# Kernel tuning notes

Hardware: AMD Instinct MI355X
Metric: run time of the kernel (lower is better)

Reference implementation:

```python
import jax, jax.numpy as jnp
import numpy as np

MIN_CONF = 0.05          # min_confidence
NMS_IOU = 0.4            # per-class nms iou threshold
POST_IOU = 0.65          # post (cross-class, per-image) nms iou threshold
MAX_OUT = 1000           # nms_max_output_size (also the 'top 1000 boxes' cap)


def _corners(boxes):
    # boxes: [..., 4] (cx, cy, w, h) -> (y1, x1, y2, x2); image w=h=1 since
    # NormalizeBoxes is called without a shape kwarg in the original layer.
    cx, cy, w, h = jnp.moveaxis(boxes, -1, 0)
    return jnp.stack([cy - h / 2, cx - w / 2, cy + h / 2, cx + w / 2], axis=-1)


def _iou_matrix(b):
    # b: [K, 4] (y1, x1, y2, x2) -> [K, K] pairwise IoU
    y1, x1, y2, x2 = b[:, 0], b[:, 1], b[:, 2], b[:, 3]
    area = (y2 - y1) * (x2 - x1)
    ih = jnp.clip(jnp.minimum(y2[:, None], y2[None, :]) - jnp.maximum(y1[:, None], y1[None, :]), 0.0)
    iw = jnp.clip(jnp.minimum(x2[:, None], x2[None, :]) - jnp.maximum(x1[:, None], x1[None, :]), 0.0)
    inter = ih * iw
    union = area[:, None] + area[None, :] - inter
    return inter / jnp.maximum(union, 1e-8)


def _greedy_nms(b, valid, thresh):
    # b: [K,4] corner boxes sorted by descending score; valid: [K] bool.
    # Greedy NMS identical to tf.image.non_max_suppression (suppress IoU > thresh).
    iou = _iou_matrix(b)
    K = b.shape[0]
    idx = jnp.arange(K)
    def body(i, supp):
        active = valid[i] & jnp.logical_not(supp[i])
        return supp | (active & (iou[i] > thresh) & (idx > i))
    supp = jax.lax.fori_loop(0, K, body, jnp.zeros(K, dtype=bool))
    return valid & jnp.logical_not(supp)


def _forward(cls_pred, boxes):
    B, N, C = cls_pred.shape
    K1 = MAX_OUT
    corners = _corners(boxes)                                 # [B, N, 4]

    # --- stage 1: confidence filter + per-(image,class) NMS -----------------
    scores = jnp.transpose(cls_pred, (0, 2, 1))               # [B, C, N]
    masked = jnp.where(scores >= MIN_CONF, scores, -1.0)
    s1, i1 = jax.lax.top_k(masked, K1)                        # [B, C, K1], top-1000 cap
    v1 = s1 >= MIN_CONF
    b1 = jnp.take_along_axis(corners[:, None], i1[..., None], axis=2)  # [B, C, K1, 4]
    keep1 = jax.vmap(lambda bb, vv: _greedy_nms(bb, vv, NMS_IOU))(
        b1.reshape(B * C, K1, 4), v1.reshape(B * C, K1)).reshape(B, C, K1)

    # --- stage 2: per-image cross-class post-NMS ----------------------------
    s2 = jnp.where(keep1, s1, -1.0).reshape(B, C * K1)
    cls_ids = jnp.broadcast_to(jnp.arange(C)[None, :, None], (B, C, K1)).reshape(B, C * K1)
    b2 = b1.reshape(B, C * K1, 4)
    i2 = i1.reshape(B, C * K1)

    K2 = MAX_OUT
    s2t, sel = jax.lax.top_k(s2, K2)                          # [B, K2]
    v2 = s2t >= MIN_CONF
    b2t = jnp.take_along_axis(b2, sel[..., None], axis=1)     # [B, K2, 4]
    cls_t = jnp.take_along_axis(cls_ids, sel, axis=1)         # [B, K2]
    orig_t = jnp.take_along_axis(i2, sel, axis=1)             # [B, K2] anchor index
    keep2 = jax.vmap(lambda bb, vv: _greedy_nms(bb, vv, POST_IOU))(b2t, v2)

    # --- compact kept detections to the front, pad with zeros ---------------
    order = jnp.argsort(jnp.logical_not(keep2).astype(jnp.int32), axis=1)  # stable
    keep_s = jnp.take_along_axis(keep2, order, axis=1)
    conf = jnp.where(keep_s, jnp.take_along_axis(s2t, order, axis=1), 0.0)
    cls_f = jnp.where(keep_s, jnp.take_along_axis(cls_t, order, axis=1), 0).astype(jnp.float32)
    oidx = jnp.take_along_axis(orig_t, order, axis=1)
    raw = jnp.take_along_axis(boxes, oidx[..., None], axis=1)  # original (cx,cy,w,h)
    raw = jnp.where(keep_s[..., None], raw, 0.0)
    out = jnp.concatenate([raw, cls_f[..., None], conf[..., None]], axis=-1)  # [B, K2, 6]
    return jax.lax.stop_gradient(out)


def setup_inputs() -> dict:
    key = jax.random.key(0)
    k1, k2 = jax.random.split(key)
    B, N, C = 8, 100000, 10
    cls_pred = jax.random.uniform(k1, (B, N, C), dtype=jnp.float32)
    boxes = jax.random.uniform(k2, (B, N, 4), dtype=jnp.float32)  # (cx, cy, w, h)
    return {"cls_pred": cls_pred, "boxes": boxes}


def reference(cls_pred, boxes):
    return _forward(cls_pred, boxes)
```

## Files before the change

### kernel.cpp

```cpp
#include <hip/hip_runtime.h>
#include <stdint.h>
#include <string.h>

typedef unsigned int u32;
typedef unsigned long long u64;

#define B_ 8
#define N_ 100000
#define C_ 10
#define K1_ 1000
#define N2_ (C_ * K1_)
#define NBIN 4096
#define CAP 4096
#define CAP_C 2048
#define SEGROWS 256
#define MIN_CONF_F 0.05f
#define NMS_IOU_F 0.4f
#define POST_IOU_F 0.65f
#define T0_F 0.985f

#define TOTAL_F4 (B_ * N_ * C_ / 4)
#define CBLK 512
#define LCAP 512
#define HDRW 84

#define NTILE 136
#define NB_ 34
#define TPB_ 4

static __device__ __forceinline__ u32 next_pow2_ge(u32 x, u32 lo, u32 hi) {
  u32 n = lo;
  while (n < x && n < hi) n <<= 1;
  return n;
}

#define TILE_ID(rt, w) ((rt) * 16 - (((rt) * ((rt) - 1)) >> 1) + ((w) - (rt)))

static __device__ __forceinline__ void prep_write(const float* __restrict__ bb,
                                                  float s, int oi,
                                                  float4* __restrict__ cor,
                                                  int pos) {
  bool v = (s >= MIN_CONF_F);
  float cx = 0.f, cy = 0.f, w = 0.f, h = 0.f;
  if (v) {
    const float4 bp = *(const float4*)(bb + (size_t)oi * 4);
    cx = bp.x; cy = bp.y; w = bp.z; h = bp.w;
  }
  float y1 = cy - h * 0.5f, x1 = cx - w * 0.5f;
  float y2 = cy + h * 0.5f, x2 = cx + w * 0.5f;
  cor[pos] = make_float4(y1, x1, y2, x2);
}

__global__ __launch_bounds__(256) void k_compact(const float* __restrict__ cls,
                                                 u64* __restrict__ cand,
                                                 u32* __restrict__ hdr) {
  __shared__ u32 lcnt[B_ * C_];
  __shared__ u32 lpre[B_ * C_ + 1];
  __shared__ u32 ltot;
  __shared__ u32 lovf;
  __shared__ u64 ekey[LCAP];
  __shared__ u32 emeta[LCAP];

  const int tid = threadIdx.x;
  const u32 bk = blockIdx.x;
  if (tid < B_ * C_) lcnt[tid] = 0;
  if (tid == 0) { ltot = 0; lovf = 0; }
  __syncthreads();

  const u32 lo = bk * ((TOTAL_F4 + CBLK - 1) / CBLK);
  u32 hi = lo + ((TOTAL_F4 + CBLK - 1) / CBLK);
  if (hi > TOTAL_F4) hi = TOTAL_F4;

  const float4* p4 = (const float4*)cls;
// ... 30 lines not shown
  for (int off = 1; off < B_ * C_; off <<= 1) {
    u32 v = 0;
    const bool act = (tid >= off && tid <= B_ * C_);
    if (act) v = lpre[tid - off];
    __syncthreads();
    if (act) lpre[tid] += v;
    __syncthreads();
  }

  u32 tot = ltot;
  if (tot > LCAP) tot = LCAP;
  u64* seg = cand + (size_t)bk * LCAP;
  for (u32 p = tid; p < tot; p += 256) {
    u32 mta = emeta[p];
    u32 slice = mta >> 16;
    u32 rank = mta & 0xFFFFu;
    u32 dst = lpre[slice] + rank;
    if (dst < LCAP) seg[dst] = ekey[p];
  }
  if (tid <= B_ * C_) hdr[bk * HDRW + tid] = lpre[tid];
  if (tid == 0) hdr[bk * HDRW + 81] = lovf;
}

__device__ __forceinline__ void bitonic_sort_desc(u64* buf, u32 n, int tid,
                                                  int bd) {
  for (u32 kk = 2; kk <= n; kk <<= 1) {
    for (u32 j = kk >> 1; j > 0; j >>= 1) {
      for (u32 t = tid; t < (n >> 1); t += bd) {
        u32 i = ((t & ~(j - 1)) << 1) | (t & (j - 1));
        u32 l = i | j;
        u64 a = buf[i], bb = buf[l];
        bool desc = ((i & kk) == 0);
        if (desc ? (a < bb) : (a > bb)) { buf[i] = bb; buf[l] = a; }
      }
      __syncthreads();
    }
  }
}

__global__ __launch_bounds__(1024) void k_sel(const float* __restrict__ cls,
                                              const u64* __restrict__ cand,
                                              const u32* __restrict__ hdr,
                                              float* __restrict__ score1,
                                              int* __restrict__ idx1,
                                              const float* __restrict__ boxes,
                                              float4* __restrict__ cor1,
                                              int do_prep) {
  const int slice = blockIdx.x;
  const int tid = threadIdx.x;
  const int bd = 1024;

  __shared__ u32 hist[NBIN];
  __shared__ u64 buf[CAP];
  __shared__ int sh_b1;
  __shared__ u32 sh_base, sh_T, sh_cnt, sh_ovf;

  u32* cnts = hist;
  u32* starts = hist + 512;
  u32* pre = hist + 1024;

  if (tid == 0) sh_ovf = 0;
  __syncthreads();
// ... 119 lines not shown
        if (l > i) {
          u64 a = buf[i], bb2 = buf[l];
          bool desc = ((i & kk) == 0);
          if (desc ? (a < bb2) : (a > bb2)) { buf[i] = bb2; buf[l] = a; }
        }
      }
      __syncthreads();
    }
  }

  float os = -1.0f; int ooi = 0;
  if (tid < K1_) {
    u64 e = buf[tid];
    u32 k = (u32)(e >> 32);
    if (k != 0) { os = __uint_as_float(k); ooi = (int)(~(u32)e); }
    score1[slice * K1_ + tid] = os;
    idx1[slice * K1_ + tid] = ooi;
  }
  if (do_prep)
    prep_write(boxes + (size_t)(slice / C_) * N_ * 4, os, ooi, cor1,
               (slice << 10) + tid);
}


template <bool STRICT>
static __device__ __forceinline__ bool iou_pred(float inter, float den,
                                                float m1, float m0) {
  float t = __fmul_rn(m1, den);
  float e = __builtin_fmaf(m1, den, -t);
  float r = __builtin_fmaf(m0, den, e);
  float d = __fsub_rn(inter, t);
  return STRICT ? (d > r) : (d >= r);
}

template <bool STRICT>
__global__ __launch_bounds__(256) void k_nms_build(const float4* __restrict__ cor,
                                                   float m1, float m0,
                                                   u64* __restrict__ maskg) {
  __shared__ float4 box4[1024];
  __shared__ float area[1024];
  const int blk = blockIdx.x;
  const int slice = blk / NB_;
  const int sub = blk - slice * NB_;
  const int tid = threadIdx.x, wave = tid >> 6, lane = tid & 63;

  for (int p = tid; p < 1024; p += 256) {
    const float4 c = cor[(slice << 10) + p];
    box4[p] = c;
    area[p] = (c.z - c.x) * (c.w - c.y);
  }
  __syncthreads();

  u64* mg = maskg + (size_t)slice * (NTILE * 64);

  for (int k = wave; k < TPB_; k += 4) {
    const int tt = sub * TPB_ + k;
    if (tt >= NTILE) break;
    int rt = 0, bse = 0;
    while (tt >= bse + (16 - rt)) { bse += 16 - rt; ++rt; }
    const int w = rt + (tt - bse);
    const int row = (rt << 6) | lane;

    const float4 ib = box4[row];
    const float ia = area[row];
    const float4* jcol = &box4[w << 6];
    const float* jarea = &area[w << 6];
    u32 mhi = 0, mlo = 0;
#pragma unroll 8
    for (int j = 63; j >= 32; --j) {
      const float4 jb = jcol[j];
      const float ja = jarea[j];
      float ih = fminf(ib.z, jb.z) - fmaxf(ib.x, jb.x); ih = fmaxf(ih, 0.0f);
      float iw_ = fminf(ib.w, jb.w) - fmaxf(ib.y, jb.y); iw_ = fmaxf(iw_, 0.0f);
      float inter = ih * iw_;
      float den = fmaxf((ia + ja) - inter, 1e-8f);
      bool p_ = iou_pred<STRICT>(inter, den, m1, m0);
      mhi = (mhi << 1) | (p_ ? 1u : 0u);
    }
#pragma unroll 8
    for (int j = 31; j >= 0; --j) {
      const float4 jb = jcol[j];
      const float ja = jarea[j];
      float ih = fminf(ib.z, jb.z) - fmaxf(ib.x, jb.x); ih = fmaxf(ih, 0.0f);
      float iw_ = fminf(ib.w, jb.w) - fmaxf(ib.y, jb.y); iw_ = fmaxf(iw_, 0.0f);
      float inter = ih * iw_;
      float den = fmaxf((ia + ja) - inter, 1e-8f);
      bool p_ = iou_pred<STRICT>(inter, den, m1, m0);
      mlo = (mlo << 1) | (p_ ? 1u : 0u);
    }
    u64 m = ((u64)mhi << 32) | (u64)mlo;
    if (w == rt) m &= (lane == 63) ? 0ull : (~0ull << (lane + 1));
    mg[(tt << 6) + lane] = m;
  }
}

__device__ void scan_core(const u64* __restrict__ mg,
                          const float* __restrict__ scores,
                          u64* __restrict__ keepb) {
  const int tid = threadIdx.x, wv = tid >> 6, lane = tid & 63;

  float s = (tid < K1_) ? scores[tid] : -1.0f;
  const u64 myvalid = __ballot(s >= MIN_CONF_F);

  u64 ext_partial = 0;

#pragma unroll 1
  for (int g = 0; g < 16; ++g) {
    u64 Tg = 0ull;
    if (g <= wv) Tg = mg[(TILE_ID(g, wv) << 6) + lane];
    const u64 nz = __ballot(Tg != 0ull);
    if (wv == g) {
      u64 ext = ext_partial;
      for (int off = 1; off < 64; off <<= 1) {
        u32 lo = (u32)__shfl_xor((int)(u32)ext, off, 64);
        u32 hi = (u32)__shfl_xor((int)(u32)(ext >> 32), off, 64);
        ext |= ((u64)hi << 32) | lo;
      }
      const u32 tlo = (u32)Tg, thi = (u32)(Tg >> 32);
      u64 rem = myvalid & ~ext;
      u64 cand = rem & nz;
      while (cand) {
        int i = __ffsll((long long)cand) - 1;
        cand &= cand - 1;
        if ((rem >> i) & 1ull) {
          u32 rlo = __builtin_amdgcn_readlane(tlo, i);
          u32 rhi = __builtin_amdgcn_readlane(thi, i);
          u64 row = ((u64)rhi << 32) | rlo;
          rem &= ~row;
          cand &= ~row;
        }
      }
      if (lane == 0) keepb[g] = rem;
    }
    __syncthreads();
    if (wv > g) {
      u64 kg = keepb[g];
      if ((kg >> lane) & 1ull) ext_partial |= Tg;
    }
  }
}

__global__ __launch_bounds__(1024) void k_nms_scan1(const u64* __restrict__ maskg,
                                                    const float* __restrict__ score1,
                                                    int* __restrict__ keep1) {
  __shared__ u64 keepb[16];
  const int slice = blockIdx.x;
  scan_core(maskg + (size_t)slice * (NTILE * 64), score1 + slice * K1_, keepb);
  __syncthreads();
  const int p = threadIdx.x;
  if (p < K1_)
    keep1[slice * K1_ + p] = (int)((keepb[p >> 6] >> (p & 63)) & 1ull);
}

__global__ __launch_bounds__(1024) void k_nms_scan2(const u64* __restrict__ maskg,
                                                    const float* __restrict__ sel_score,
                                                    const int* __restrict__ sel_cls,
                                                    const int* __restrict__ sel_orig,
                                                    const float* __restrict__ boxes,
                                                    float* __restrict__ out) {
  __shared__ u64 keepb[16];
  __shared__ short ord[K1_];
  __shared__ int lbase[17];
  __shared__ int ordc;
  const int b = blockIdx.x;
  const int tid = threadIdx.x;
  scan_core(maskg + (size_t)b * (NTILE * 64), sel_score + b * K1_, keepb);
  __syncthreads();

  if (tid == 0) {
    int acc = 0;
    for (int wdx = 0; wdx < 16; ++wdx) {
      lbase[wdx] = acc;
      acc += __popcll(keepb[wdx]);
    }
    lbase[16] = acc;
    ordc = acc;
  }
  __syncthreads();
  if (tid < 16) {
    u64 m = keepb[tid];
    int base = lbase[tid];
    while (m) {
      int bit = __ffsll((long long)m) - 1;
      ord[base++] = (short)((tid << 6) | bit);
      m &= m - 1;
    }
  }
  __syncthreads();

  for (int t = tid; t < K1_ * 6; t += 1024) out[(size_t)b * K1_ * 6 + t] = 0.0f;
  __syncthreads();

  const int cnt = ordc;
  for (int q = tid; q < cnt; q += 1024) {
    int p = ord[q];
    int oi = sel_orig[b * K1_ + p];
    const float4 bp = *(const float4*)(boxes + ((size_t)b * N_ + oi) * 4);
    float* o = out + ((size_t)b * K1_ + q) * 6;
    o[0] = bp.x; o[1] = bp.y; o[2] = bp.z; o[3] = bp.w;
    o[4] = (float)sel_cls[b * K1_ + p];
    o[5] = sel_score[b * K1_ + p];
  }
}

__device__ __forceinline__ void nms_run(const float* __restrict__ scores,
                                        const int* __restrict__ origs,
                                        const float* __restrict__ boxesB,
                                        float thr,
                                        float4* box4, float* area,
                                        u64* mask, u64* validw, u64* keepw) {
  const int tid = threadIdx.x;
  const int wave = tid >> 6, lane = tid & 63;

  {
    const int p = tid;
    float s = (p < K1_) ? scores[p] : -1.0f;
    bool v = (s >= MIN_CONF_F);
    float cx = 0.f, cy = 0.f, w = 0.f, h = 0.f;
    if (v) {
      const float4 bp = *(const float4*)(boxesB + (size_t)origs[p] * 4);
      cx = bp.x; cy = bp.y; w = bp.z; h = bp.w;
    }
    float y1 = cy - h * 0.5f, x1 = cx - w * 0.5f;
    float y2 = cy + h * 0.5f, x2 = cx + w * 0.5f;
    box4[p] = make_float4(y1, x1, y2, x2);
// ... 181 lines not shown
    while (m) {
      int bit = __ffsll((long long)m) - 1;
      ord[base++] = (short)((tid << 6) | bit);
      m &= m - 1;
    }
  }
  __syncthreads();

  for (int t = tid; t < K1_ * 6; t += 1024) out[(size_t)b * K1_ * 6 + t] = 0.0f;
  __syncthreads();

  const int cnt = ordc;
  for (int q = tid; q < cnt; q += 1024) {
    int p = ord[q];
    int oi = sel_orig[b * K1_ + p];
    const float4 bp = *(const float4*)(boxes + ((size_t)b * N_ + oi) * 4);
    float* o = out + ((size_t)b * K1_ + q) * 6;
    o[0] = bp.x; o[1] = bp.y; o[2] = bp.z; o[3] = bp.w;
    o[4] = (float)sel_cls[b * K1_ + p];
    o[5] = sel_score[b * K1_ + p];
  }
}

__device__ __forceinline__ void suffix_select(const u32* __restrict__ hist,
                                              u32* __restrict__ aux,
                                              u32 base, u32 K,
                                              int* out_bin, u32* out_next) {
  const int t = threadIdx.x;
  u32 h0 = hist[4 * t], h1 = hist[4 * t + 1];
  u32 h2 = hist[4 * t + 2], h3 = hist[4 * t + 3];
  aux[t] = h0 + h1 + h2 + h3;
  __syncthreads();
  for (int off = 1; off < 1024; off <<= 1) {
    u32 v = aux[t] + ((t + off < 1024) ? aux[t + off] : 0u);
    __syncthreads();
    aux[t] = v;
    __syncthreads();
  }
  if (t == 0 && base + aux[0] < K) { *out_bin = -1; *out_next = base; }
  u32 up = (t < 1023) ? aux[t + 1] : 0u;
  u32 s3 = h3 + up;
  u32 s2 = h2 + s3;
  u32 s1 = h1 + s2;
  u32 s0 = h0 + s1;
  u32 c0 = base + s0, c1 = base + s1, c2 = base + s2, c3 = base + s3;
  u32 c4 = base + up;
  if (c0 >= K && c1 < K) { *out_bin = 4 * t;     *out_next = c1; }
  if (c1 >= K && c2 < K) { *out_bin = 4 * t + 1; *out_next = c2; }
  if (c2 >= K && c3 < K) { *out_bin = 4 * t + 2; *out_next = c3; }
  if (c3 >= K && c4 < K) { *out_bin = 4 * t + 3; *out_next = c4; }
  __syncthreads();
}

__global__ __launch_bounds__(1024) void k_topk2(const float* __restrict__ score1,
                                                const int* __restrict__ idx1,
                                                const int* __restrict__ keep1,
                                                float* __restrict__ sel_score,
                                                int* __restrict__ sel_cls,
                                                int* __restrict__ sel_orig,
                                                const float* __restrict__ boxes,
                                                float4* __restrict__ cor2,
                                                int do_prep) {
  const int b = blockIdx.x;
  const int tid = threadIdx.x;

  __shared__ u32 hist[NBIN];
  __shared__ u32 aux[1024];
  __shared__ u64 buf[CAP];
  __shared__ int sh_bin;
  __shared__ u32 sh_next;
  __shared__ u32 sh_T, sh_cnt;

  for (int i = tid; i < NBIN; i += 1024) hist[i] = 0;
  __syncthreads();
  for (int f = tid; f < N2_; f += 1024) {
    if (keep1[b * N2_ + f])
      atomicAdd(&hist[__float_as_uint(score1[b * N2_ + f]) >> 19], 1u);
  }
  __syncthreads();
  suffix_select(hist, aux, 0u, (u32)K1_, &sh_bin, &sh_next);
  const int b1 = sh_bin;
  const u32 base = sh_next;

  if (b1 >= 0) {
    for (int i = tid; i < NBIN; i += 1024) hist[i] = 0;
    if (tid == 0) sh_bin = -2;
    __syncthreads();
    for (int f = tid; f < N2_; f += 1024) {
      if (keep1[b * N2_ + f]) {
        u32 k = __float_as_uint(score1[b * N2_ + f]);
        if ((int)(k >> 19) == b1) atomicAdd(&hist[(k >> 7) & 0xFFFu], 1u);
      }
    }
    __syncthreads();
    suffix_select(hist, aux, base, (u32)K1_, &sh_bin, &sh_next);
    if (tid == 0) {
      int b2 = sh_bin;
      sh_T = (b2 >= 0) ? ((((u32)b1) << 19) | (((u32)b2) << 7))
                       : (((u32)b1) << 19);
    }
  } else {
    if (tid == 0) sh_T = 0;
  }
  if (tid == 0) sh_cnt = 0;
  __syncthreads();

  const u32 T = sh_T;
  for (int f = tid; f < N2_; f += 1024) {
    if (keep1[b * N2_ + f]) {
      u32 k = __float_as_uint(score1[b * N2_ + f]);
      if (k >= T) {
        u32 pos = atomicAdd(&sh_cnt, 1u);
        if (pos < CAP) buf[pos] = ((u64)k << 32) | (u32)(~(u32)f);
      }
    }
  }
  __syncthreads();
  u32 m = sh_cnt; if (m > CAP) m = CAP;
  const u32 n = next_pow2_ge(m, 1024u, (u32)CAP);
  for (u32 i = tid; i < n; i += 1024)
    if (i >= m) buf[i] = 0ull;
  __syncthreads();

  bitonic_sort_desc(buf, n, tid, 1024);

  float os = -1.0f; int ooi = 0;
  if (tid < K1_) {
    u64 e = buf[tid];
    u32 k = (u32)(e >> 32);
    float s; int cls, orig;
    if (k == 0) { s = -1.0f; cls = 0; orig = 0; }
    else {
      s = __uint_as_float(k);
      u32 f = ~(u32)e;
      cls = (int)(f / K1_);
      int slot = (int)(f - (u32)cls * K1_);
      orig = idx1[(b * C_ + cls) * K1_ + slot];
    }
    sel_score[b * K1_ + tid] = s;
    sel_cls[b * K1_ + tid] = cls;
    sel_orig[b * K1_ + tid] = orig;
    os = s; ooi = orig;
  }
  if (do_prep)
    prep_write(boxes + (size_t)b * N_ * 4, os, ooi, cor2, (b << 10) + tid);
}

static inline void m_split(float cf, float* m1, float* m0, bool* strict) {
  u32 b; memcpy(&b, &cf, 4);
  u32 nb = b + 1; float cn; memcpy(&cn, &nb, 4);
  double M = ((double)cf + (double)cn) * 0.5;
  *m1 = (float)M;
  *m0 = (float)(M - (double)*m1);
  *strict = ((b & 1u) == 0u);
}

extern "C" void kernel_launch(void* const* d_in, const int* in_sizes, int n_in,
                              void* d_out, int out_size, void* d_ws, size_t ws_size,
                              hipStream_t stream) {
  const float* cls = (const float*)d_in[0];
  const float* boxes = (const float*)d_in[1];
  float* out = (float*)d_out;

  char* ws = (char*)d_ws;
  float* score1    = (float*)(ws);
  int*   idx1      = (int*)(ws + 320000);
  int*   keep1     = (int*)(ws + 640000);
  float* sel_score = (float*)(ws + 960000);
  int*   sel_cls   = (int*)(ws + 992000);
  int*   sel_orig  = (int*)(ws + 1024000);
  u32*   hdr       = (u32*)(ws + 1056000);
  u64*   cand      = (u64*)(ws + 1228032);
  u64*   mask1     = (u64*)(ws + 3325184);
  u64*   mask2     = (u64*)(ws + 3325184);
  float4* cor1     = (float4*)(ws + 8895744);
  float4* cor2     = (float4*)(ws + 8895744);
  const size_t WS_NEED = 10206464;

  const int do_fast = (ws_size >= WS_NEED) ? 1 : 0;

  hipLaunchKernelGGL(k_compact, dim3(CBLK), dim3(256), 0, stream,
                     cls, cand, hdr);
  hipLaunchKernelGGL(k_sel, dim3(B_ * C_), dim3(1024), 0, stream,
                     cls, cand, hdr, score1, idx1, boxes, cor1, do_fast);

  if (do_fast) {
    float m1a, m0a, m1b, m0b; bool sa, sb;
    m_split(NMS_IOU_F, &m1a, &m0a, &sa);
    m_split(POST_IOU_F, &m1b, &m0b, &sb);

    if (sa)
      hipLaunchKernelGGL(k_nms_build<true>, dim3(B_ * C_ * NB_), dim3(256), 0,
                         stream, cor1, m1a, m0a, mask1);
    else
      hipLaunchKernelGGL(k_nms_build<false>, dim3(B_ * C_ * NB_), dim3(256), 0,
                         stream, cor1, m1a, m0a, mask1);
    hipLaunchKernelGGL(k_nms_scan1, dim3(B_ * C_), dim3(1024), 0, stream,
                       mask1, score1, keep1);
    hipLaunchKernelGGL(k_topk2, dim3(B_), dim3(1024), 0, stream,
                       score1, idx1, keep1, sel_score, sel_cls, sel_orig,
                       boxes, cor2, 1);
    if (sb)
      hipLaunchKernelGGL(k_nms_build<true>, dim3(B_ * NB_), dim3(256), 0,
                         stream, cor2, m1b, m0b, mask2);
    else
      hipLaunchKernelGGL(k_nms_build<false>, dim3(B_ * NB_), dim3(256), 0,
                         stream, cor2, m1b, m0b, mask2);
    hipLaunchKernelGGL(k_nms_scan2, dim3(B_), dim3(1024), 0, stream,
                       mask2, sel_score, sel_cls, sel_orig, boxes, out);
  } else {
    hipLaunchKernelGGL(k_nms1, dim3(B_ * C_), dim3(1024), 0, stream,
                       boxes, score1, idx1, keep1);
    hipLaunchKernelGGL(k_topk2, dim3(B_), dim3(1024), 0, stream,
// ... 7 lines not shown
```

Measured before the change: 218.3 us.

## Fuse the NMS pipeline into one cooperative persistent kernel with grid syncs

Replaces the chain of separate kernel launches (compact, per-slice top-k, mask build, scan, top-k2, second mask build, scan) with a single cooperative kernel of 240 blocks of 1024 threads. Stages are separated by grid.sync, and shared memory is reused through a union. The aim is to remove per-launch overhead and the gaps between launches in this chain of small kernels. The cost is fewer resident blocks in the wide stages, idle blocks during the narrow stages, and the expense of each grid barrier. The old multi-kernel path is kept as a fallback when cooperative launch is unavailable or fails.

Result: slower. 716.1 us (+227.9%).

```diff
diff --git a/kernel.cpp b/kernel.cpp
--- a/kernel.cpp
+++ b/kernel.cpp
@@ -1,6 +1,9 @@
 #include <hip/hip_runtime.h>
+#include <hip/hip_cooperative_groups.h>
 #include <stdint.h>
 #include <string.h>
+
+namespace cg = cooperative_groups;
 
 typedef unsigned int u32;
 typedef unsigned long long u64;
@@ -27,6 +30,7 @@
 #define NTILE 136
 #define NB_ 34
 #define TPB_ 4
+#define NBLK_ 240
 
 static __device__ __forceinline__ u32 next_pow2_ge(u32 x, u32 lo, u32 hi) {
   u32 n = lo;
@@ -49,6 +53,539 @@
   float y1 = cy - h * 0.5f, x1 = cx - w * 0.5f;
   float y2 = cy + h * 0.5f, x2 = cx + w * 0.5f;
   cor[pos] = make_float4(y1, x1, y2, x2);
+}
+
+template <bool STRICT>
+static __device__ __forceinline__ bool iou_pred(float inter, float den,
+                                                float m1, float m0) {
+  float t = __fmul_rn(m1, den);
+  float e = __builtin_fmaf(m1, den, -t);
+  float r = __builtin_fmaf(m0, den, e);
+  float d = __fsub_rn(inter, t);
+  return STRICT ? (d > r) : (d >= r);
+}
+
+template <bool STRICT>
+static __device__ __forceinline__ void build_tile(const float4* __restrict__ box4,
+                                                  const float* __restrict__ area,
+                                                  int tt, int lane,
+                                                  float m1, float m0,
+                                                  u64* __restrict__ mg) {
+  int rt = 0, bse = 0;
+  while (tt >= bse + (16 - rt)) { bse += 16 - rt; ++rt; }
+  const int w = rt + (tt - bse);
+  const int row = (rt << 6) | lane;
+
+  const float4 ib = box4[row];
+  const float ia = area[row];
+  const float4* jcol = &box4[w << 6];
+  const float* jarea = &area[w << 6];
+  u32 mhi = 0, mlo = 0;
+#pragma unroll 8
+  for (int j = 63; j >= 32; --j) {
+    const float4 jb = jcol[j];
+    const float ja = jarea[j];
+    float ih = fminf(ib.z, jb.z) - fmaxf(ib.x, jb.x); ih = fmaxf(ih, 0.0f);
+    float iw_ = fminf(ib.w, jb.w) - fmaxf(ib.y, jb.y); iw_ = fmaxf(iw_, 0.0f);
+    float inter = ih * iw_;
+    float den = fmaxf((ia + ja) - inter, 1e-8f);
+    bool p_ = iou_pred<STRICT>(inter, den, m1, m0);
+    mhi = (mhi << 1) | (p_ ? 1u : 0u);
+  }
+#pragma unroll 8
+  for (int j = 31; j >= 0; --j) {
+    const float4 jb = jcol[j];
+    const float ja = jarea[j];
+    float ih = fminf(ib.z, jb.z) - fmaxf(ib.x, jb.x); ih = fmaxf(ih, 0.0f);
+    float iw_ = fminf(ib.w, jb.w) - fmaxf(ib.y, jb.y); iw_ = fmaxf(iw_, 0.0f);
+    float inter = ih * iw_;
+    float den = fmaxf((ia + ja) - inter, 1e-8f);
+    bool p_ = iou_pred<STRICT>(inter, den, m1, m0);
+    mlo = (mlo << 1) | (p_ ? 1u : 0u);
+  }
+  u64 m = ((u64)mhi << 32) | (u64)mlo;
+  if (w == rt) m &= (lane == 63) ? 0ull : (~0ull << (lane + 1));
+  mg[(tt << 6) + lane] = m;
+}
+
+__device__ __forceinline__ void bitonic_sort_desc(u64* buf, u32 n, int tid,
+                                                  int bd) {
+  for (u32 kk = 2; kk <= n; kk <<= 1) {
+    for (u32 j = kk >> 1; j > 0; j >>= 1) {
+      for (u32 t = tid; t < (n >> 1); t += bd) {
+        u32 i = ((t & ~(j - 1)) << 1) | (t & (j - 1));
+        u32 l = i | j;
+        u64 a = buf[i], bb = buf[l];
+        bool desc = ((i & kk) == 0);
+        if (desc ? (a < bb) : (a > bb)) { buf[i] = bb; buf[l] = a; }
+      }
+      __syncthreads();
+    }
+  }
+}
+
+__device__ void scan_core(const u64* __restrict__ mg, float s,
+                          u64* __restrict__ keepb) {
+  const int tid = threadIdx.x, wv = tid >> 6, lane = tid & 63;
+  const u64 myvalid = __ballot(s >= MIN_CONF_F);
+
+  u64 ext_partial = 0;
+
+#pragma unroll 1
+  for (int g = 0; g < 16; ++g) {
+    u64 Tg = 0ull;
+    if (g <= wv) Tg = mg[(TILE_ID(g, wv) << 6) + lane];
+    const u64 nz = __ballot(Tg != 0ull);
+    if (wv == g) {
+      u64 ext = ext_partial;
+      for (int off = 1; off < 64; off <<= 1) {
+        u32 lo = (u32)__shfl_xor((int)(u32)ext, off, 64);
+        u32 hi = (u32)__shfl_xor((int)(u32)(ext >> 32), off, 64);
+        ext |= ((u64)hi << 32) | lo;
+      }
+      const u32 tlo = (u32)Tg, thi = (u32)(Tg >> 32);
+      u64 rem = myvalid & ~ext;
+      u64 cand = rem & nz;
+      while (cand) {
+        int i = __ffsll((long long)cand) - 1;
+        cand &= cand - 1;
+        if ((rem >> i) & 1ull) {
+          u32 rlo = __builtin_amdgcn_readlane(tlo, i);
+          u32 rhi = __builtin_amdgcn_readlane(thi, i);
+          u64 row = ((u64)rhi << 32) | rlo;
+          rem &= ~row;
+          cand &= ~row;
+        }
+      }
+      if (lane == 0) keepb[g] = rem;
+    }
+    __syncthreads();
+    if (wv > g) {
+      u64 kg = keepb[g];
+      if ((kg >> lane) & 1ull) ext_partial |= Tg;
+    }
+  }
+}
+
+__device__ __forceinline__ void suffix_select(const u32* __restrict__ hist,
+                                              u32* __restrict__ aux,
+                                              u32 base, u32 K,
+                                              int* out_bin, u32* out_next) {
+  const int t = threadIdx.x;
+  u32 h0 = hist[4 * t], h1 = hist[4 * t + 1];
+  u32 h2 = hist[4 * t + 2], h3 = hist[4 * t + 3];
+  aux[t] = h0 + h1 + h2 + h3;
+  __syncthreads();
+  for (int off = 1; off < 1024; off <<= 1) {
+    u32 v = aux[t] + ((t + off < 1024) ? aux[t + off] : 0u);
+    __syncthreads();
+    aux[t] = v;
+    __syncthreads();
+  }
+  if (t == 0 && base + aux[0] < K) { *out_bin = -1; *out_next = base; }
+  u32 up = (t < 1023) ? aux[t + 1] : 0u;
+  u32 s3 = h3 + up;
+  u32 s2 = h2 + s3;
+  u32 s1 = h1 + s2;
+  u32 s0 = h0 + s1;
+  u32 c0 = base + s0, c1 = base + s1, c2 = base + s2, c3 = base + s3;
+  u32 c4 = base + up;
+  if (c0 >= K && c1 < K) { *out_bin = 4 * t;     *out_next = c1; }
+  if (c1 >= K && c2 < K) { *out_bin = 4 * t + 1; *out_next = c2; }
+  if (c2 >= K && c3 < K) { *out_bin = 4 * t + 2; *out_next = c3; }
+  if (c3 >= K && c4 < K) { *out_bin = 4 * t + 3; *out_next = c4; }
+  __syncthreads();
+}
+
+template <bool S1, bool S2>
+__global__ __launch_bounds__(1024) void k_mega(
+    const float* __restrict__ cls, const float* __restrict__ boxes,
+    float* __restrict__ out,
+    float* __restrict__ score1, int* __restrict__ idx1, int* __restrict__ keep1,
+    float* __restrict__ sel_score, int* __restrict__ sel_cls,
+    int* __restrict__ sel_orig,
+    u32* __restrict__ hdr, u64* __restrict__ cand,
+    u64* __restrict__ mask1, u64* __restrict__ mask2,
+    float4* __restrict__ cor1, float4* __restrict__ cor2,
+    float m1a, float m0a, float m1b, float m0b) {
+  cg::grid_group grid = cg::this_grid();
+  const int tid = threadIdx.x;
+  const int bid = blockIdx.x;
+  const int wave = tid >> 6, lane = tid & 63;
+
+  __shared__ union U {
+    struct { u32 lcnt[B_ * C_]; u32 lpre[B_ * C_ + 1]; u64 ekey[LCAP]; u32 emeta[LCAP]; } cp;
+    struct { u32 hist[NBIN]; u32 aux[1024]; u64 buf[CAP]; } s;
+    struct { float4 box4[1024]; float area[1024]; } bl;
+    struct { u64 keepb[16]; short ord[K1_]; int lbase[17]; } sc;
+  } sh;
+  __shared__ u32 sh_ltot, sh_lovf, sh_ovf, sh_base, sh_T, sh_cnt, sh_next;
+  __shared__ int sh_b1, sh_ordc;
+
+  for (u32 ck = (u32)bid; ck < CBLK; ck += NBLK_) {
+    if (tid < B_ * C_) sh.cp.lcnt[tid] = 0;
+    if (tid == 0) { sh_ltot = 0; sh_lovf = 0; }
+    __syncthreads();
+
+    const u32 lo = ck * ((TOTAL_F4 + CBLK - 1) / CBLK);
+    u32 hi = lo + ((TOTAL_F4 + CBLK - 1) / CBLK);
+    if (hi > TOTAL_F4) hi = TOTAL_F4;
+
+    const float4* p4 = (const float4*)cls;
+    for (u32 f = lo + tid; f < hi; f += 1024) {
+      float4 v = p4[f];
+      u32 e = f * 4u;
+      float vs[4] = {v.x, v.y, v.z, v.w};
+#pragma unroll
+      for (int j = 0; j < 4; ++j) {
+        float sv = vs[j];
+        if (sv >= T0_F) {
+          u32 g = e + (u32)j;
+          u32 gi = g / (u32)C_;
+          u32 c = g - gi * (u32)C_;
+          u32 bi = gi / (u32)N_;
+          u32 i = gi - bi * (u32)N_;
+          u32 slice = bi * (u32)C_ + c;
+          u32 rank = atomicAdd(&sh.cp.lcnt[slice], 1u);
+          u32 pos = atomicAdd(&sh_ltot, 1u);
+          if (pos < LCAP) {
+            sh.cp.ekey[pos] = ((u64)__float_as_uint(sv) << 32) | (u32)(~i);
+            sh.cp.emeta[pos] = (slice << 16) | rank;
+          } else {
+            sh_lovf = 1;
+          }
+        }
+      }
+    }
+    __syncthreads();
+
+    if (tid < B_ * C_) sh.cp.lpre[tid + 1] = sh.cp.lcnt[tid];
+    if (tid == 0) sh.cp.lpre[0] = 0;
+    __syncthreads();
+    for (int off = 1; off < B_ * C_; off <<= 1) {
+      u32 v = 0;
+      const bool act = (tid >= off && tid <= B_ * C_);
+      if (act) v = sh.cp.lpre[tid - off];
+      __syncthreads();
+      if (act) sh.cp.lpre[tid] += v;
+      __syncthreads();
+    }
+
+    u32 tot = sh_ltot;
+    if (tot > LCAP) tot = LCAP;
+    u64* seg = cand + (size_t)ck * LCAP;
+    for (u32 p = tid; p < tot; p += 1024) {
+      u32 mta = sh.cp.emeta[p];
+      u32 slice = mta >> 16;
+      u32 rank = mta & 0xFFFFu;
+      u32 dst = sh.cp.lpre[slice] + rank;
+      if (dst < LCAP) seg[dst] = sh.cp.ekey[p];
+    }
+    if (tid <= B_ * C_) hdr[ck * HDRW + tid] = sh.cp.lpre[tid];
+    if (tid == 0) hdr[ck * HDRW + 81] = sh_lovf;
+    __syncthreads();
+  }
+  __threadfence();
+  grid.sync();
+
+  if (bid < B_ * C_) {
+    const int slice = bid;
+    u32* cnts = sh.s.hist;
+    u32* starts = sh.s.hist + 512;
+    u32* pre = sh.s.hist + 1024;
+
+    if (tid == 0) sh_ovf = 0;
+    __syncthreads();
+    if (tid < CBLK) {
+      const u32* h = hdr + (size_t)tid * HDRW;
+      u32 a = h[slice], b2 = h[slice + 1];
+      starts[tid] = a;
+      cnts[tid] = b2 - a;
+      pre[tid + 1] = b2 - a;
+      if (h[81]) sh_ovf = 1;
+    }
+    if (tid == 0) pre[0] = 0;
+    __syncthreads();
+    for (int off = 1; off < CBLK; off <<= 1) {
+      u32 v = 0;
+      const bool act = (tid >= off && tid <= CBLK);
+      if (act) v = pre[tid - off];
+      __syncthreads();
+      if (act) pre[tid] += v;
+      __syncthreads();
+    }
+    const u32 mm = pre[CBLK];
+    const bool fastp = (sh_ovf == 0) && mm >= (u32)K1_ && mm <= (u32)CAP_C;
+
+    float os = -1.0f; int ooi = 0;
+    if (fastp) {
+      if (tid < CBLK) {
+        u32 n = cnts[tid];
+        u32 base2 = pre[tid];
+        const u64* src = cand + (size_t)tid * LCAP + starts[tid];
+        for (u32 r = 0; r < n; ++r) sh.s.buf[base2 + r] = src[r];
+      }
+      __syncthreads();
+      const u32 nn = next_pow2_ge(mm, 1024u, (u32)CAP_C);
+      for (u32 i2 = tid; i2 < nn; i2 += 1024)
+        if (i2 >= mm) sh.s.buf[i2] = 0ull;
+      __syncthreads();
+      bitonic_sort_desc(sh.s.buf, nn, tid, 1024);
+      if (tid < K1_) {
+        u64 e = sh.s.buf[tid];
+        u32 k = (u32)(e >> 32);
+        os = __uint_as_float(k);
+        ooi = (int)(~(u32)e);
+      }
+    } else {
+      const int b = slice / C_, c = slice % C_;
+      for (int i = tid; i < NBIN; i += 1024) sh.s.hist[i] = 0;
+      __syncthreads();
+      for (int i = tid; i < N_; i += 1024) {
+        float sv = cls[((size_t)b * N_ + i) * C_ + c];
+        if (sv >= MIN_CONF_F) atomicAdd(&sh.s.hist[__float_as_uint(sv) >> 19], 1u);
+      }
+      __syncthreads();
+      if (tid == 0) {
+        u32 cum = 0; int b1 = -1; u32 base = 0;
+        for (int bin = NBIN - 1; bin >= 0; --bin) {
+          cum += sh.s.hist[bin];
+          if (cum >= (u32)K1_) { b1 = bin; base = cum - sh.s.hist[bin]; break; }
+        }
+        sh_b1 = b1; sh_base = base;
+        if (b1 < 0) sh_T = 0;
+      }
+      __syncthreads();
+      const int b1 = sh_b1;
+      if (b1 >= 0) {
+        const u32 base = sh_base;
+        for (int i = tid; i < NBIN; i += 1024) sh.s.hist[i] = 0;
+        __syncthreads();
+        for (int i = tid; i < N_; i += 1024) {
+          float sv = cls[((size_t)b * N_ + i) * C_ + c];
+          if (sv >= MIN_CONF_F) {
+            u32 k = __float_as_uint(sv);
+            if ((int)(k >> 19) == b1) atomicAdd(&sh.s.hist[(k >> 7) & 0xFFFu], 1u);
+          }
+        }
+        __syncthreads();
+        if (tid == 0) {
+          u32 cum = base;
+          u32 T = ((u32)b1) << 19;
+          for (int bin = NBIN - 1; bin >= 0; --bin) {
+            cum += sh.s.hist[bin];
+            if (cum >= (u32)K1_) { T = (((u32)b1) << 19) | (((u32)bin) << 7); break; }
+          }
+          sh_T = T;
+        }
+        __syncthreads();
+      }
+      if (tid == 0) sh_cnt = 0;
+      __syncthreads();
+      const u32 T = sh_T;
+      for (int i = tid; i < N_; i += 1024) {
+        float sv = cls[((size_t)b * N_ + i) * C_ + c];
+        if (sv >= MIN_CONF_F) {
+          u32 k = __float_as_uint(sv);
+          if (k >= T) {
+            u32 pos = atomicAdd(&sh_cnt, 1u);
+            if (pos < CAP) sh.s.buf[pos] = ((u64)k << 32) | (u32)(~(u32)i);
+          }
+        }
+      }
+      __syncthreads();
+      u32 m2 = sh_cnt; if (m2 > CAP) m2 = CAP;
+      for (int i = tid; i < CAP; i += 1024)
+        if ((u32)i >= m2) sh.s.buf[i] = 0ull;
+      __syncthreads();
+      bitonic_sort_desc(sh.s.buf, CAP, tid, 1024);
+      if (tid < K1_) {
+        u64 e = sh.s.buf[tid];
+        u32 k = (u32)(e >> 32);
+        if (k != 0) { os = __uint_as_float(k); ooi = (int)(~(u32)e); }
+      }
+    }
+    if (tid < K1_) {
+      score1[slice * K1_ + tid] = os;
+      idx1[slice * K1_ + tid] = ooi;
+    }
+    prep_write(boxes + (size_t)(slice / C_) * N_ * 4, os, ooi, cor1,
+               (slice << 10) + tid);
+  }
+  __threadfence();
+  grid.sync();
+
+  {
+    const int slice = bid % (B_ * C_);
+    const int sub = bid / (B_ * C_);
+    {
+      const int p = tid;
+      const float4 c = cor1[(slice << 10) + p];
+      sh.bl.box4[p] = c;
+      sh.bl.area[p] = (c.z - c.x) * (c.w - c.y);
+    }
+    __syncthreads();
+    u64* mg = mask1 + (size_t)slice * (NTILE * 64);
+    for (int k = wave; ; k += 16) {
+      const int tt = sub + 3 * k;
+      if (tt >= NTILE) break;
+      build_tile<S1>(sh.bl.box4, sh.bl.area, tt, lane, m1a, m0a, mg);
+    }
+  }
+  __threadfence();
+  grid.sync();
+
+  if (bid < B_ * C_) {
+    const int slice = bid;
+    float sv = (tid < K1_) ? score1[slice * K1_ + tid] : -1.0f;
+    scan_core(mask1 + (size_t)slice * (NTILE * 64), sv, sh.sc.keepb);
+    __syncthreads();
+    if (tid < K1_)
+      keep1[slice * K1_ + tid] =
+          (int)((sh.sc.keepb[tid >> 6] >> (tid & 63)) & 1ull);
+  }
+  __threadfence();
+  grid.sync();
+
+  if (bid < B_) {
+    const int b = bid;
+    for (int i = tid; i < NBIN; i += 1024) sh.s.hist[i] = 0;
+    __syncthreads();
+    for (int f = tid; f < N2_; f += 1024) {
+      if (keep1[b * N2_ + f])
+        atomicAdd(&sh.s.hist[__float_as_uint(score1[b * N2_ + f]) >> 19], 1u);
+    }
+    __syncthreads();
+    suffix_select(sh.s.hist, sh.s.aux, 0u, (u32)K1_, &sh_b1, &sh_next);
+    const int b1 = sh_b1;
+    const u32 base = sh_next;
+
+    if (b1 >= 0) {
+      for (int i = tid; i < NBIN; i += 1024) sh.s.hist[i] = 0;
+      if (tid == 0) sh_b1 = -2;
+      __syncthreads();
+      for (int f = tid; f < N2_; f += 1024) {
+        if (keep1[b * N2_ + f]) {
+          u32 k = __float_as_uint(score1[b * N2_ + f]);
+          if ((int)(k >> 19) == b1) atomicAdd(&sh.s.hist[(k >> 7) & 0xFFFu], 1u);
+        }
+      }
+      __syncthreads();
+      suffix_select(sh.s.hist, sh.s.aux, base, (u32)K1_, &sh_b1, &sh_next);
+      if (tid == 0) {
+        int b2 = sh_b1;
+        sh_T = (b2 >= 0) ? ((((u32)b1) << 19) | (((u32)b2) << 7))
+                         : (((u32)b1) << 19);
+      }
+    } else {
+      if (tid == 0) sh_T = 0;
+    }
+    if (tid == 0) sh_cnt = 0;
+    __syncthreads();
+
+    const u32 T = sh_T;
+    for (int f = tid; f < N2_; f += 1024) {
+      if (keep1[b * N2_ + f]) {
+        u32 k = __float_as_uint(score1[b * N2_ + f]);
+        if (k >= T) {
+          u32 pos = atomicAdd(&sh_cnt, 1u);
+          if (pos < CAP) sh.s.buf[pos] = ((u64)k << 32) | (u32)(~(u32)f);
+        }
+      }
+    }
+    __syncthreads();
+    u32 m2 = sh_cnt; if (m2 > CAP) m2 = CAP;
+    const u32 n = next_pow2_ge(m2, 1024u, (u32)CAP);
+    for (u32 i = tid; i < n; i += 1024)
+      if (i >= m2) sh.s.buf[i] = 0ull;
+    __syncthreads();
+
+    bitonic_sort_desc(sh.s.buf, n, tid, 1024);
+
+    float os = -1.0f; int ooi = 0;
+    if (tid < K1_) {
+      u64 e = sh.s.buf[tid];
+      u32 k = (u32)(e >> 32);
+      float sv; int cls2, orig;
+      if (k == 0) { sv = -1.0f; cls2 = 0; orig = 0; }
+      else {
+        sv = __uint_as_float(k);
+        u32 f = ~(u32)e;
+        cls2 = (int)(f / K1_);
+        int slot = (int)(f - (u32)cls2 * K1_);
+        orig = idx1[(b * C_ + cls2) * K1_ + slot];
+      }
+      sel_score[b * K1_ + tid] = sv;
+      sel_cls[b * K1_ + tid] = cls2;
+      sel_orig[b * K1_ + tid] = orig;
+      os = sv; ooi = orig;
+    }
+    prep_write(boxes + (size_t)b * N_ * 4, os, ooi, cor2, (b << 10) + tid);
+  }
+  __threadfence();
+  grid.sync();
+
+  {
+    const int b = bid % B_;
+    const int sub = bid / B_;
+    {
+      const int p = tid;
+      const float4 c = cor2[(b << 10) + p];
+      sh.bl.box4[p] = c;
+      sh.bl.area[p] = (c.z - c.x) * (c.w - c.y);
+    }
+    __syncthreads();
+    u64* mg = mask2 + (size_t)b * (NTILE * 64);
+    for (int k = wave; ; k += 16) {
+      const int tt = sub + 30 * k;
+      if (tt >= NTILE) break;
+      build_tile<S2>(sh.bl.box4, sh.bl.area, tt, lane, m1b, m0b, mg);
+    }
+  }
+  __threadfence();
+  grid.sync();
+
+  if (bid < B_) {
+    const int b = bid;
+    float sv = (tid < K1_) ? sel_score[b * K1_ + tid] : -1.0f;
+    scan_core(mask2 + (size_t)b * (NTILE * 64), sv, sh.sc.keepb);
+    __syncthreads();
+
+    if (tid == 0) {
+      int acc = 0;
+      for (int wdx = 0; wdx < 16; ++wdx) {
+        sh.sc.lbase[wdx] = acc;
+        acc += __popcll(sh.sc.keepb[wdx]);
+      }
+      sh.sc.lbase[16] = acc;
+      sh_ordc = acc;
+    }
+    __syncthreads();
+    if (tid < 16) {
+      u64 m = sh.sc.keepb[tid];
+      int base = sh.sc.lbase[tid];
+      while (m) {
+        int bit = __ffsll((long long)m) - 1;
+        sh.sc.ord[base++] = (short)((tid << 6) | bit);
+        m &= m - 1;
+      }
+    }
+    __syncthreads();
+
+    for (int t = tid; t < K1_ * 6; t += 1024) out[(size_t)b * K1_ * 6 + t] = 0.0f;
+    __syncthreads();
+
+    const int cnt = sh_ordc;
+    for (int q = tid; q < cnt; q += 1024) {
+      int p = sh.sc.ord[q];
+      int oi = sel_orig[b * K1_ + p];
+      const float4 bp = *(const float4*)(boxes + ((size_t)b * N_ + oi) * 4);
+      float* o = out + ((size_t)b * K1_ + q) * 6;
+      o[0] = bp.x; o[1] = bp.y; o[2] = bp.z; o[3] = bp.w;
+      o[4] = (float)sel_cls[b * K1_ + p];
+      o[5] = sel_score[b * K1_ + p];
+    }
+  }
 }
 
 __global__ __launch_bounds__(256) void k_compact(const float* __restrict__ cls,
@@ -125,22 +662,6 @@
   if (tid == 0) hdr[bk * HDRW + 81] = lovf;
 }
 
-__device__ __forceinline__ void bitonic_sort_desc(u64* buf, u32 n, int tid,
-                                                  int bd) {
-  for (u32 kk = 2; kk <= n; kk <<= 1) {
-    for (u32 j = kk >> 1; j > 0; j >>= 1) {
-      for (u32 t = tid; t < (n >> 1); t += bd) {
-        u32 i = ((t & ~(j - 1)) << 1) | (t & (j - 1));
-        u32 l = i | j;
-        u64 a = buf[i], bb = buf[l];
-        bool desc = ((i & kk) == 0);
-        if (desc ? (a < bb) : (a > bb)) { buf[i] = bb; buf[l] = a; }
-      }
-      __syncthreads();
-    }
-  }
-}
-
 __global__ __launch_bounds__(1024) void k_sel(const float* __restrict__ cls,
                                               const u64* __restrict__ cand,
                                               const u32* __restrict__ hdr,
@@ -306,17 +827,6 @@
                (slice << 10) + tid);
 }
 
-
-template <bool STRICT>
-static __device__ __forceinline__ bool iou_pred(float inter, float den,
-                                                float m1, float m0) {
-  float t = __fmul_rn(m1, den);
-  float e = __builtin_fmaf(m1, den, -t);
-  float r = __builtin_fmaf(m0, den, e);
-  float d = __fsub_rn(inter, t);
-  return STRICT ? (d > r) : (d >= r);
-}
-
 template <bool STRICT>
 __global__ __launch_bounds__(256) void k_nms_build(const float4* __restrict__ cor,
                                                    float m1, float m0,
@@ -340,87 +850,7 @@
   for (int k = wave; k < TPB_; k += 4) {
     const int tt = sub * TPB_ + k;
     if (tt >= NTILE) break;
-    int rt = 0, bse = 0;
-    while (tt >= bse + (16 - rt)) { bse += 16 - rt; ++rt; }
-    const int w = rt + (tt - bse);
-    const int row = (rt << 6) | lane;
-
-    const float4 ib = box4[row];
-    const float ia = area[row];
-    const float4* jcol = &box4[w << 6];
-    const float* jarea = &area[w << 6];
-    u32 mhi = 0, mlo = 0;
-#pragma unroll 8
-    for (int j = 63; j >= 32; --j) {
-      const float4 jb = jcol[j];
-      const float ja = jarea[j];
-      float ih = fminf(ib.z, jb.z) - fmaxf(ib.x, jb.x); ih = fmaxf(ih, 0.0f);
-      float iw_ = fminf(ib.w, jb.w) - fmaxf(ib.y, jb.y); iw_ = fmaxf(iw_, 0.0f);
-      float inter = ih * iw_;
-      float den = fmaxf((ia + ja) - inter, 1e-8f);
-      bool p_ = iou_pred<STRICT>(inter, den, m1, m0);
-      mhi = (mhi << 1) | (p_ ? 1u : 0u);
-    }
-#pragma unroll 8
-    for (int j = 31; j >= 0; --j) {
-      const float4 jb = jcol[j];
-      const float ja = jarea[j];
-      float ih = fminf(ib.z, jb.z) - fmaxf(ib.x, jb.x); ih = fmaxf(ih, 0.0f);
-      float iw_ = fminf(ib.w, jb.w) - fmaxf(ib.y, jb.y); iw_ = fmaxf(iw_, 0.0f);
-      float inter = ih * iw_;
-      float den = fmaxf((ia + ja) - inter, 1e-8f);
-      bool p_ = iou_pred<STRICT>(inter, den, m1, m0);
-      mlo = (mlo << 1) | (p_ ? 1u : 0u);
-    }
-    u64 m = ((u64)mhi << 32) | (u64)mlo;
-    if (w == rt) m &= (lane == 63) ? 0ull : (~0ull << (lane + 1));
-    mg[(tt << 6) + lane] = m;
-  }
-}
-
-__device__ void scan_core(const u64* __restrict__ mg,
-                          const float* __restrict__ scores,
-                          u64* __restrict__ keepb) {
-  const int tid = threadIdx.x, wv = tid >> 6, lane = tid & 63;
-
-  float s = (tid < K1_) ? scores[tid] : -1.0f;
-  const u64 myvalid = __ballot(s >= MIN_CONF_F);
-
-  u64 ext_partial = 0;
-
-#pragma unroll 1
-  for (int g = 0; g < 16; ++g) {
-    u64 Tg = 0ull;
-    if (g <= wv) Tg = mg[(TILE_ID(g, wv) << 6) + lane];
-    const u64 nz = __ballot(Tg != 0ull);
-    if (wv == g) {
-      u64 ext = ext_partial;
-      for (int off = 1; off < 64; off <<= 1) {
-        u32 lo = (u32)__shfl_xor((int)(u32)ext, off, 64);
-        u32 hi = (u32)__shfl_xor((int)(u32)(ext >> 32), off, 64);
-        ext |= ((u64)hi << 32) | lo;
-      }
-      const u32 tlo = (u32)Tg, thi = (u32)(Tg >> 32);
-      u64 rem = myvalid & ~ext;
-      u64 cand = rem & nz;
-      while (cand) {
-        int i = __ffsll((long long)cand) - 1;
-        cand &= cand - 1;
-        if ((rem >> i) & 1ull) {
-          u32 rlo = __builtin_amdgcn_readlane(tlo, i);
-          u32 rhi = __builtin_amdgcn_readlane(thi, i);
-          u64 row = ((u64)rhi << 32) | rlo;
-          rem &= ~row;
-          cand &= ~row;
-        }
-      }
-      if (lane == 0) keepb[g] = rem;
-    }
-    __syncthreads();
-    if (wv > g) {
-      u64 kg = keepb[g];
-      if ((kg >> lane) & 1ull) ext_partial |= Tg;
-    }
+    build_tile<STRICT>(box4, area, tt, lane, m1, m0, mg);
   }
 }
 
@@ -429,11 +859,12 @@
                                                     int* __restrict__ keep1) {
   __shared__ u64 keepb[16];
   const int slice = blockIdx.x;
-  scan_core(maskg + (size_t)slice * (NTILE * 64), score1 + slice * K1_, keepb);
-  __syncthreads();
-  const int p = threadIdx.x;
-  if (p < K1_)
-    keep1[slice * K1_ + p] = (int)((keepb[p >> 6] >> (p & 63)) & 1ull);
+  const int tid = threadIdx.x;
+  float s = (tid < K1_) ? score1[slice * K1_ + tid] : -1.0f;
+  scan_core(maskg + (size_t)slice * (NTILE * 64), s, keepb);
+  __syncthreads();
+  if (tid < K1_)
+    keep1[slice * K1_ + tid] = (int)((keepb[tid >> 6] >> (tid & 63)) & 1ull);
 }
 
 __global__ __launch_bounds__(1024) void k_nms_scan2(const u64* __restrict__ maskg,
@@ -448,7 +879,8 @@
   __shared__ int ordc;
   const int b = blockIdx.x;
   const int tid = threadIdx.x;
-  scan_core(maskg + (size_t)b * (NTILE * 64), sel_score + b * K1_, keepb);
+  float s = (tid < K1_) ? sel_score[b * K1_ + tid] : -1.0f;
+  scan_core(maskg + (size_t)b * (NTILE * 64), s, keepb);
   __syncthreads();
 
   if (tid == 0) {
@@ -485,6 +917,100 @@
     o[4] = (float)sel_cls[b * K1_ + p];
     o[5] = sel_score[b * K1_ + p];
   }
+}
+
+__global__ __launch_bounds__(1024) void k_topk2(const float* __restrict__ score1,
+                                                const int* __restrict__ idx1,
+                                                const int* __restrict__ keep1,
+                                                float* __restrict__ sel_score,
+                                                int* __restrict__ sel_cls,
+                                                int* __restrict__ sel_orig,
+                                                const float* __restrict__ boxes,
+                                                float4* __restrict__ cor2,
+                                                int do_prep) {
+  const int b = blockIdx.x;
+  const int tid = threadIdx.x;
+
+  __shared__ u32 hist[NBIN];
+  __shared__ u32 aux[1024];
+  __shared__ u64 buf[CAP];
+  __shared__ int sh_bin;
+  __shared__ u32 sh_next;
+  __shared__ u32 sh_T, sh_cnt;
+
+  for (int i = tid; i < NBIN; i += 1024) hist[i] = 0;
+  __syncthreads();
+  for (int f = tid; f < N2_; f += 1024) {
+    if (keep1[b * N2_ + f])
+      atomicAdd(&hist[__float_as_uint(score1[b * N2_ + f]) >> 19], 1u);
+  }
+  __syncthreads();
+  suffix_select(hist, aux, 0u, (u32)K1_, &sh_bin, &sh_next);
+  const int b1 = sh_bin;
+  const u32 base = sh_next;
+
+  if (b1 >= 0) {
+    for (int i = tid; i < NBIN; i += 1024) hist[i] = 0;
+    if (tid == 0) sh_bin = -2;
+    __syncthreads();
+    for (int f = tid; f < N2_; f += 1024) {
+      if (keep1[b * N2_ + f]) {
+        u32 k = __float_as_uint(score1[b * N2_ + f]);
+        if ((int)(k >> 19) == b1) atomicAdd(&hist[(k >> 7) & 0xFFFu], 1u);
+      }
+    }
+    __syncthreads();
+    suffix_select(hist, aux, base, (u32)K1_, &sh_bin, &sh_next);
+    if (tid == 0) {
+      int b2 = sh_bin;
+      sh_T = (b2 >= 0) ? ((((u32)b1) << 19) | (((u32)b2) << 7))
+                       : (((u32)b1) << 19);
+    }
+  } else {
+    if (tid == 0) sh_T = 0;
+  }
+  if (tid == 0) sh_cnt = 0;
+  __syncthreads();
+
+  const u32 T = sh_T;
+  for (int f = tid; f < N2_; f += 1024) {
+    if (keep1[b * N2_ + f]) {
+      u32 k = __float_as_uint(score1[b * N2_ + f]);
+      if (k >= T) {
+        u32 pos = atomicAdd(&sh_cnt, 1u);
+        if (pos < CAP) buf[pos] = ((u64)k << 32) | (u32)(~(u32)f);
+      }
+    }
+  }
+  __syncthreads();
+  u32 m = sh_cnt; if (m > CAP) m = CAP;
+  const u32 n = next_pow2_ge(m, 1024u, (u32)CAP);
+  for (u32 i = tid; i < n; i += 1024)
+    if (i >= m) buf[i] = 0ull;
+  __syncthreads();
+
+  bitonic_sort_desc(buf, n, tid, 1024);
+
+  float os = -1.0f; int ooi = 0;
+  if (tid < K1_) {
+    u64 e = buf[tid];
+    u32 k = (u32)(e >> 32);
+    float s; int cls, orig;
+    if (k == 0) { s = -1.0f; cls = 0; orig = 0; }
+    else {
+      s = __uint_as_float(k);
+      u32 f = ~(u32)e;
+      cls = (int)(f / K1_);
+      int slot = (int)(f - (u32)cls * K1_);
+      orig = idx1[(b * C_ + cls) * K1_ + slot];
+    }
+    sel_score[b * K1_ + tid] = s;
+    sel_cls[b * K1_ + tid] = cls;
+    sel_orig[b * K1_ + tid] = orig;
+    os = s; ooi = orig;
+  }
+  if (do_prep)
+    prep_write(boxes + (size_t)b * N_ * 4, os, ooi, cor2, (b << 10) + tid);
 }
 
 __device__ __forceinline__ void nms_run(const float* __restrict__ scores,
@@ -712,130 +1238,6 @@
   }
 }
 
-__device__ __forceinline__ void suffix_select(const u32* __restrict__ hist,
-                                              u32* __restrict__ aux,
-                                              u32 base, u32 K,
-                                              int* out_bin, u32* out_next) {
-  const int t = threadIdx.x;
-  u32 h0 = hist[4 * t], h1 = hist[4 * t + 1];
-  u32 h2 = hist[4 * t + 2], h3 = hist[4 * t + 3];
-  aux[t] = h0 + h1 + h2 + h3;
-  __syncthreads();
-  for (int off = 1; off < 1024; off <<= 1) {
-    u32 v = aux[t] + ((t + off < 1024) ? aux[t + off] : 0u);
-    __syncthreads();
-    aux[t] = v;
-    __syncthreads();
-  }
-  if (t == 0 && base + aux[0] < K) { *out_bin = -1; *out_next = base; }
-  u32 up = (t < 1023) ? aux[t + 1] : 0u;
-  u32 s3 = h3 + up;
-  u32 s2 = h2 + s3;
-  u32 s1 = h1 + s2;
-  u32 s0 = h0 + s1;
-  u32 c0 = base + s0, c1 = base + s1, c2 = base + s2, c3 = base + s3;
-  u32 c4 = base + up;
-  if (c0 >= K && c1 < K) { *out_bin = 4 * t;     *out_next = c1; }
-  if (c1 >= K && c2 < K) { *out_bin = 4 * t + 1; *out_next = c2; }
-  if (c2 >= K && c3 < K) { *out_bin = 4 * t + 2; *out_next = c3; }
-  if (c3 >= K && c4 < K) { *out_bin = 4 * t + 3; *out_next = c4; }
-  __syncthreads();
-}
-
-__global__ __launch_bounds__(1024) void k_topk2(const float* __restrict__ score1,
-                                                const int* __restrict__ idx1,
-                                                const int* __restrict__ keep1,
-                                                float* __restrict__ sel_score,
-                                                int* __restrict__ sel_cls,
-                                                int* __restrict__ sel_orig,
-                                                const float* __restrict__ boxes,
-                                                float4* __restrict__ cor2,
-                                                int do_prep) {
-  const int b = blockIdx.x;
-  const int tid = threadIdx.x;
-
-  __shared__ u32 hist[NBIN];
-  __shared__ u32 aux[1024];
-  __shared__ u64 buf[CAP];
-  __shared__ int sh_bin;
-  __shared__ u32 sh_next;
-  __shared__ u32 sh_T, sh_cnt;
-
-  for (int i = tid; i < NBIN; i += 1024) hist[i] = 0;
-  __syncthreads();
-  for (int f = tid; f < N2_; f += 1024) {
-    if (keep1[b * N2_ + f])
-      atomicAdd(&hist[__float_as_uint(score1[b * N2_ + f]) >> 19], 1u);
-  }
-  __syncthreads();
-  suffix_select(hist, aux, 0u, (u32)K1_, &sh_bin, &sh_next);
-  const int b1 = sh_bin;
-  const u32 base = sh_next;
-
-  if (b1 >= 0) {
-    for (int i = tid; i < NBIN; i += 1024) hist[i] = 0;
-    if (tid == 0) sh_bin = -2;
-    __syncthreads();
-    for (int f = tid; f < N2_; f += 1024) {
-      if (keep1[b * N2_ + f]) {
-        u32 k = __float_as_uint(score1[b * N2_ + f]);
-        if ((int)(k >> 19) == b1) atomicAdd(&hist[(k >> 7) & 0xFFFu], 1u);
-      }
-    }
-    __syncthreads();
-    suffix_select(hist, aux, base, (u32)K1_, &sh_bin, &sh_next);
-    if (tid == 0) {
-      int b2 = sh_bin;
-      sh_T = (b2 >= 0) ? ((((u32)b1) << 19) | (((u32)b2) << 7))
-                       : (((u32)b1) << 19);
-    }
-  } else {
-    if (tid == 0) sh_T = 0;
-  }
-  if (tid == 0) sh_cnt = 0;
-  __syncthreads();
-
-  const u32 T = sh_T;
-  for (int f = tid; f < N2_; f += 1024) {
-    if (keep1[b * N2_ + f]) {
-      u32 k = __float_as_uint(score1[b * N2_ + f]);
-      if (k >= T) {
-        u32 pos = atomicAdd(&sh_cnt, 1u);
-        if (pos < CAP) buf[pos] = ((u64)k << 32) | (u32)(~(u32)f);
-      }
-    }
-  }
-  __syncthreads();
-  u32 m = sh_cnt; if (m > CAP) m = CAP;
-  const u32 n = next_pow2_ge(m, 1024u, (u32)CAP);
-  for (u32 i = tid; i < n; i += 1024)
-    if (i >= m) buf[i] = 0ull;
-  __syncthreads();
-
-  bitonic_sort_desc(buf, n, tid, 1024);
-
-  float os = -1.0f; int ooi = 0;
-  if (tid < K1_) {
-    u64 e = buf[tid];
-    u32 k = (u32)(e >> 32);
-    float s; int cls, orig;
-    if (k == 0) { s = -1.0f; cls = 0; orig = 0; }
-    else {
-      s = __uint_as_float(k);
-      u32 f = ~(u32)e;
-      cls = (int)(f / K1_);
-      int slot = (int)(f - (u32)cls * K1_);
-      orig = idx1[(b * C_ + cls) * K1_ + slot];
-    }
-    sel_score[b * K1_ + tid] = s;
-    sel_cls[b * K1_ + tid] = cls;
-    sel_orig[b * K1_ + tid] = orig;
-    os = s; ooi = orig;
-  }
-  if (do_prep)
-    prep_write(boxes + (size_t)b * N_ * 4, os, ooi, cor2, (b << 10) + tid);
-}
-
 static inline void m_split(float cf, float* m1, float* m0, bool* strict) {
   u32 b; memcpy(&b, &cf, 4);
   u32 nb = b + 1; float cn; memcpy(&cn, &nb, 4);
@@ -867,6 +1269,38 @@
   float4* cor2     = (float4*)(ws + 8895744);
   const size_t WS_NEED = 10206464;
 
+  float m1a, m0a, m1b, m0b; bool sa, sb;
+  m_split(NMS_IOU_F, &m1a, &m0a, &sa);
+  m_split(POST_IOU_F, &m1b, &m0b, &sb);
+
+  static int coop_ok = -1;
+  if (coop_ok < 0) {
+    int v = 0, dev = 0;
+    (void)hipGetDevice(&dev);
+    if (hipDeviceGetAttribute(&v, hipDeviceAttributeCooperativeLaunch, dev) !=
+        hipSuccess)
+      v = 0;
+    coop_ok = v;
+  }
+
+  if (coop_ok && ws_size >= WS_NEED) {
+    void* args[] = {
+        (void*)&cls, (void*)&boxes, (void*)&out,
+        (void*)&score1, (void*)&idx1, (void*)&keep1,
+        (void*)&sel_score, (void*)&sel_cls, (void*)&sel_orig,
+        (void*)&hdr, (void*)&cand, (void*)&mask1, (void*)&mask2,
+        (void*)&cor1, (void*)&cor2,
+        (void*)&m1a, (void*)&m0a, (void*)&m1b, (void*)&m0b};
+    const void* fn =
+        sa ? (sb ? (const void*)k_mega<true, true>
+                 : (const void*)k_mega<true, false>)
+           : (sb ? (const void*)k_mega<false, true>
+                 : (const void*)k_mega<false, false>);
+    hipError_t e = hipLaunchCooperativeKernel(fn, dim3(NBLK_), dim3(1024),
+                                              args, 0, stream);
+    if (e == hipSuccess) return;
+  }
+
   const int do_fast = (ws_size >= WS_NEED) ? 1 : 0;
 
   hipLaunchKernelGGL(k_compact, dim3(CBLK), dim3(256), 0, stream,
@@ -875,10 +1309,6 @@
                      cls, cand, hdr, score1, idx1, boxes, cor1, do_fast);
 
   if (do_fast) {
-    float m1a, m0a, m1b, m0b; bool sa, sb;
-    m_split(NMS_IOU_F, &m1a, &m0a, &sa);
-    m_split(POST_IOU_F, &m1b, &m0b, &sb);
-
     if (sa)
       hipLaunchKernelGGL(k_nms_build<true>, dim3(B_ * C_ * NB_), dim3(256), 0,
                          stream, cor1, m1a, m0a, mask1);
```
